# Kernel optimization log

Measured on AMD Instinct MI355X. Metric: run time of the kernel, lower is better.

The kernel has to match this reference:

```python
import jax, jax.numpy as jnp
import numpy as np

N = 100_000
E = 1_600_000
E_OUT = 400_000
IN_DIM = 16
HID = 128
OUT_DIM = 2
L = 6
BN_EPS = 1e-5


def setup_inputs() -> dict:
    key = jax.random.key(0)
    ks = jax.random.split(key, 8)
    x = jax.random.normal(ks[0], (N, IN_DIM), dtype=jnp.float32)
    edge_index = jax.random.randint(ks[1], (2, E), 0, N, dtype=jnp.int32)
    edge_index_out = jax.random.randint(ks[2], (2, E_OUT), 0, N, dtype=jnp.int32)
    embed_W = jax.random.normal(ks[3], (IN_DIM, HID), jnp.float32) / np.sqrt(IN_DIM)
    embed_b = jnp.zeros((HID,), jnp.float32)
    conv_W = jax.random.normal(ks[4], (L, HID, HID), jnp.float32) / np.sqrt(HID)
    conv_b = jnp.zeros((L, HID), jnp.float32)
    bn_gamma = jnp.ones((L, HID), jnp.float32)
    bn_beta = jnp.zeros((L, HID), jnp.float32)
    layer_weights = jnp.ones((L,), jnp.float32)
    fc_W = jax.random.normal(ks[5], (2 * HID, OUT_DIM), jnp.float32) / np.sqrt(2 * HID)
    fc_b = jnp.zeros((OUT_DIM,), jnp.float32)
    return dict(x=x, edge_index=edge_index, edge_index_out=edge_index_out,
                embed_W=embed_W, embed_b=embed_b, conv_W=conv_W, conv_b=conv_b,
                bn_gamma=bn_gamma, bn_beta=bn_beta, layer_weights=layer_weights,
                fc_W=fc_W, fc_b=fc_b)


def reference(x, edge_index, edge_index_out, embed_W, embed_b, conv_W, conv_b,
              bn_gamma, bn_beta, layer_weights, fc_W, fc_b):
    n = x.shape[0]
    # PyG GCNConv default: add self-loops + symmetric normalization
    loops = jnp.arange(n, dtype=edge_index.dtype)
    src = jnp.concatenate([edge_index[0], loops])
    dst = jnp.concatenate([edge_index[1], loops])
    deg = jax.ops.segment_sum(jnp.ones_like(src, jnp.float32), dst, num_segments=n)
    deg_inv_sqrt = jnp.where(deg > 0, jax.lax.rsqrt(jnp.maximum(deg, 1.0)), 0.0)
    norm = (deg_inv_sqrt[src] * deg_inv_sqrt[dst])[:, None]  # [E+N, 1]

    x_embed = x @ embed_W + embed_b  # [N, HID]
    w = jax.nn.softmax(layer_weights)  # softmax=True path

    for i in range(L):
        h = x_embed @ conv_W[i]                                   # linear
        agg = jax.ops.segment_sum(h[src] * norm, dst, num_segments=n) + conv_b[i]
        # BatchNorm1d, training mode (biased variance)
        mean = jnp.mean(agg, axis=0)
        var = jnp.mean(jnp.square(agg - mean), axis=0)
        hbn = (agg - mean) * jax.lax.rsqrt(var + BN_EPS) * bn_gamma[i] + bn_beta[i]
        x_embed = x_embed + w[i] * jax.nn.relu(hbn)               # weighted residual

    edge_repr = jnp.concatenate([x_embed[edge_index_out[0]], x_embed[edge_index_out[1]]], axis=-1)
    return edge_repr @ fc_W + fc_b
```

## Files before the change

### kernel.cpp

```cpp
#include <hip/hip_runtime.h>


#define NW 8192
#define BKT 128
#define CAP 6144
#define CHUNK 512

typedef __attribute__((ext_vector_type(8))) short short8;
typedef __attribute__((ext_vector_type(4))) float f32x4;

static __device__ __forceinline__ unsigned short f2bf(float f) {
  unsigned u = __float_as_uint(f);
  u = u + 0x7fffu + ((u >> 16) & 1u);
  return (unsigned short)(u >> 16);
}
static __device__ __forceinline__ float bf2f_lo(unsigned v) {
  return __uint_as_float(v << 16);
}
static __device__ __forceinline__ float bf2f_hi(unsigned v) {
  return __uint_as_float(v & 0xffff0000u);
}
static __device__ __forceinline__ unsigned pack_bf2(float a, float b) {
  return (unsigned)f2bf(a) | ((unsigned)f2bf(b) << 16);
}
static __device__ __forceinline__ unsigned rfl(unsigned v) {
  return (unsigned)__builtin_amdgcn_readfirstlane((int)v);
}


__global__ __launch_bounds__(256) void hist_bucket_kernel(const int* __restrict__ dst,
                                                          int* __restrict__ bcnt,
                                                          int e, int n, int nbk) {
  __shared__ int h[1024];
  int T = e + n;
  int chunk = (T + gridDim.x - 1) / gridDim.x;
  int j0 = blockIdx.x * chunk;
  int j1 = min(j0 + chunk, T);
  for (int i = threadIdx.x; i < nbk; i += 256) h[i] = 0;
  __syncthreads();
  for (int j = j0 + threadIdx.x; j < j1; j += 256) {
    int d = (j < e) ? dst[j] : (j - e);
    atomicAdd(&h[d >> 7], 1);
  }
  __syncthreads();
  for (int i = threadIdx.x; i < nbk; i += 256)
    if (h[i]) atomicAdd(&bcnt[i], h[i]);
}

__global__ __launch_bounds__(1024) void scan_buckets_kernel(const int* __restrict__ bcnt,
                                                            int* __restrict__ bbase,
                                                            int nbk, int total) {
  __shared__ int lds[1024];
  int t = threadIdx.x;
  int v = (t < nbk) ? bcnt[t] : 0;
  int val = v;
  lds[t] = val; __syncthreads();
  for (int off = 1; off < 1024; off <<= 1) {
    int x = (t >= off) ? lds[t - off] : 0;
    __syncthreads();
    val += x;
    lds[t] = val;
    __syncthreads();
  }
  if (t < nbk) bbase[t] = val - v;
  if (t == 0) bbase[nbk] = total;
}

__global__ __launch_bounds__(256) void scatter_bucket_kernel(const int* __restrict__ src,
                                                             const int* __restrict__ dst,
                                                             int* __restrict__ bfill,
                                                             unsigned* __restrict__ ebuf,
                                                             int e, int n, int nbk) {
  __shared__ int cntL[1024], baseL[1024];
  int T = e + n;
  int chunk = (T + gridDim.x - 1) / gridDim.x;
  int j0 = blockIdx.x * chunk;
  int j1 = min(j0 + chunk, T);
  for (int i = threadIdx.x; i < nbk; i += 256) cntL[i] = 0;
  __syncthreads();
  for (int j = j0 + threadIdx.x; j < j1; j += 256) {
    int d = (j < e) ? dst[j] : (j - e);
    atomicAdd(&cntL[d >> 7], 1);
  }
  __syncthreads();
  for (int i = threadIdx.x; i < nbk; i += 256) {
    int c = cntL[i];
    baseL[i] = c ? atomicAdd(&bfill[i], c) : 0;
    cntL[i] = 0;
  }
  __syncthreads();
  for (int j = j0 + threadIdx.x; j < j1; j += 256) {
    int s, d;
    if (j < e) { s = src[j]; d = dst[j]; } else { s = j - e; d = s; }
    int b = d >> 7;
    int r = atomicAdd(&cntL[b], 1);
    ebuf[baseL[b] + r] = ((unsigned)s << 7) | (unsigned)(d & 127);
  }
}

__global__ __launch_bounds__(256) void sort_bucket_kernel(const int* __restrict__ bbase,
                                                          const unsigned* __restrict__ ebuf,
                                                          int2* __restrict__ ebuf2,
                                                          int* __restrict__ rs,
                                                          float* __restrict__ dis,
                                                          int n, int total) {
  __shared__ unsigned el[CAP];
  __shared__ int hist[BKT], excl[BKT], cur[BKT], scn[BKT];
  int b = blockIdx.x, t = threadIdx.x;
  int e0 = bbase[b], e1 = bbase[b + 1];
  int sz = e1 - e0;
  bool inl = (sz <= CAP);
  if (inl)
    for (int i = t; i < sz; i += 256) el[i] = ebuf[e0 + i];
  if (t < BKT) hist[t] = 0;
  __syncthreads();
  for (int i = t; i < sz; i += 256) {
    unsigned w = inl ? el[i] : ebuf[e0 + i];
    atomicAdd(&hist[w & (BKT - 1)], 1);
  }
  __syncthreads();
  int val = (t < BKT) ? hist[t] : 0;
  if (t < BKT) scn[t] = val;
  __syncthreads();
  for (int off = 1; off < BKT; off <<= 1) {
    int x = (t >= off && t < BKT) ? scn[t - off] : 0;
    __syncthreads();
    if (t < BKT) { val += x; scn[t] = val; }
    __syncthreads();
  }
  if (t < BKT) {
    int ex = val - hist[t];
    excl[t] = ex;
    cur[t] = 0;
    int d = (b << 7) + t;
    if (d < n) {
      rs[d] = e0 + ex;
      dis[d] = rsqrtf((float)hist[t]);
    }
  }
  if (b == 0 && t == 0) rs[n] = total;
  __syncthreads();
  for (int i = t; i < sz; i += 256) {
    unsigned w = inl ? el[i] : ebuf[e0 + i];
    int dl = (int)(w & (BKT - 1));
    int pos = atomicAdd(&cur[dl], 1);
    ebuf2[e0 + excl[dl] + pos] = make_int2((int)(w >> 7), (b << 7) | dl);
  }
}

__global__ void norm_kernel(const int2* __restrict__ ebuf2, const float* __restrict__ dis,
                            int2* __restrict__ esn, int T) {
  int j = blockIdx.x * blockDim.x + threadIdx.x;
  if (j >= T) return;
  int2 p = ebuf2[j];
  float nm = dis[p.x] * dis[p.y];
  unsigned bits = __float_as_uint(nm) & 0xfffffffeu;
  if (j + 1 == T || ebuf2[j + 1].y != p.y) bits |= 1u;
  esn[j] = make_int2(p.x, (int)bits);
}

__global__ void misc_kernel(const int* __restrict__ rs, int* __restrict__ A,
                            int n, int nw, int eb, int wbBlocks,
                            const float* __restrict__ W, unsigned short* __restrict__ Wt,
                            int wtotal, int wtBlocks,
                            const float* __restrict__ lw, float* __restrict__ wsm, int l) {
  int b = blockIdx.x;
  if (b < wbBlocks) {
    int w = b * 256 + threadIdx.x;
    if (w > nw) return;
    int target = w * eb;
    int lo = 0, hi = n;
    while (lo < hi) {
      int mid = (lo + hi) >> 1;
      if (rs[mid] < target) lo = mid + 1; else hi = mid;
    }
    A[w] = lo;
  } else if (b < wbBlocks + wtBlocks) {
    int t = (b - wbBlocks) * 256 + threadIdx.x;
    if (t >= wtotal) return;
    int ll = t >> 14;
    int nc = (t >> 7) & 127;
    int kk = t & 127;
    Wt[t] = f2bf(W[(size_t)ll * 16384 + kk * 128 + nc]);
  } else if (threadIdx.x == 0) {
    float m = lw[0];
    for (int i = 1; i < l; ++i) m = fmaxf(m, lw[i]);
    float s = 0.f;
    for (int i = 0; i < l; ++i) s += expf(lw[i] - m);
    for (int i = 0; i < l; ++i) wsm[i] = expf(lw[i] - m) / s;
  }
}


__global__ __launch_bounds__(256) void embed_kernel(const float* __restrict__ x,
                                                    const float* __restrict__ W,
                                                    const float* __restrict__ b,
                                                    unsigned short* __restrict__ xe16, int n) {
  __shared__ float xs[64][20];
  int tid = threadIdx.x;
  int c = tid & 127, half = tid >> 7;
  float wreg[16];
#pragma unroll
  for (int k = 0; k < 16; ++k) wreg[k] = W[k * 128 + c];
  float bc = b[c];
  int ntile = (n + 63) >> 6;
  for (int t = blockIdx.x; t < ntile; t += gridDim.x) {
    int row0 = t * 64;
    {
      int r = tid >> 2, q = tid & 3;
      int row = row0 + r;
      float4 v = (row < n) ? *(const float4*)(x + (size_t)row * 16 + q * 4)
                           : make_float4(0.f, 0.f, 0.f, 0.f);
      *(float4*)&xs[r][q * 4] = v;
    }
    __syncthreads();
    int rbase = half * 32;
    for (int rr = 0; rr < 32; ++rr) {
      int row = row0 + rbase + rr;
      if (row >= n) break;
      float acc = bc;
#pragma unroll
      for (int k = 0; k < 16; ++k) acc = fmaf(xs[rbase + rr][k], wreg[k], acc);
      xe16[(size_t)row * 128 + c] = f2bf(acc);
    }
    __syncthreads();
  }
}


#define EPS 132

template<bool HASBN>
__global__ __launch_bounds__(256) void gemm_fused_kernel(
    const unsigned* __restrict__ aggbf,
    const float* __restrict__ stats8,
    const float* __restrict__ gamma, const float* __restrict__ beta,
    const float* __restrict__ wsm, int layer,
    unsigned* __restrict__ xe16,
    const unsigned short* __restrict__ Wt,
    unsigned char* __restrict__ Hq,
    float* __restrict__ hscale, int n) {
  __shared__ short8 wlds[2048];
  __shared__ unsigned short ep[64 * EPS];
  __shared__ float sc_s[128], sh_s[128];
  int tid = threadIdx.x;
  const short* WtS = (const short*)Wt;
#pragma unroll
  for (int it = 0; it < 8; ++it) {
    int s = it * 256 + tid;
    int ln = s & 63, g = s >> 6;
    int col = ((g >> 2) << 4) + (ln & 15);
    wlds[s] = *(const short8*)(WtS + (size_t)col * 128 + (g & 3) * 32 + (ln >> 4) * 8);
  }
  if (HASBN && tid < 128) {
    float s = 0.f, q = 0.f;
#pragma unroll
    for (int k = 0; k < 8; ++k) {
      s += stats8[k * 256 + tid];
      q += stats8[k * 256 + 128 + tid];
    }
    float invn = 1.f / (float)n;
    float mean = s * invn;
    float var = q * invn - mean * mean;
    float sc = gamma[tid] * rsqrtf(var + 1e-5f);
    sc_s[tid] = sc;
    sh_s[tid] = beta[tid] - mean * sc;
  }
  __syncthreads();

  int wid = tid >> 6, lane = tid & 63;
  int lrow = lane & 15, lk = lane >> 4;
  float wres = HASBN ? wsm[layer] : 0.f;

  int ntiles = (n + 63) >> 6;
  for (int tile = blockIdx.x; tile < ntiles; tile += gridDim.x) {
    int row = tile * 64 + wid * 16 + lrow;
    short8 afrag[4];
    if (row < n) {
      if (HASBN) {
        const unsigned* arow = aggbf + (size_t)row * 64;
        unsigned* xrow = xe16 + (size_t)row * 64;
#pragma unroll
        for (int ks = 0; ks < 4; ++ks) {
          int c0 = ks * 32 + lk * 8;
          uint4 av = *(const uint4*)(arow + (c0 >> 1));
          uint4 xw = *(const uint4*)(xrow + (c0 >> 1));
          unsigned aw[4] = {av.x, av.y, av.z, av.w};
          unsigned xv[4] = {xw.x, xw.y, xw.z, xw.w};
          unsigned xo[4];
          short8 af;
#pragma unroll
          for (int d = 0; d < 4; ++d) {
            int c = c0 + 2 * d;
            float v0 = fmaxf(fmaf(bf2f_lo(aw[d]), sc_s[c], sh_s[c]), 0.f);
            float v1 = fmaxf(fmaf(bf2f_hi(aw[d]), sc_s[c + 1], sh_s[c + 1]), 0.f);
            float xn0 = fmaf(wres, v0, bf2f_lo(xv[d]));
            float xn1 = fmaf(wres, v1, bf2f_hi(xv[d]));
            unsigned pw = pack_bf2(xn0, xn1);
            xo[d] = pw;
            af[2 * d]     = (short)(pw & 0xffff);
            af[2 * d + 1] = (short)(pw >> 16);
          }
          *(uint4*)(xrow + (c0 >> 1)) = make_uint4(xo[0], xo[1], xo[2], xo[3]);
          afrag[ks] = af;
        }
      } else {
        const short* AS = (const short*)xe16;
#pragma unroll
        for (int ks = 0; ks < 4; ++ks)
          afrag[ks] = *(const short8*)(AS + (size_t)row * 128 + ks * 32 + lk * 8);
      }
    } else {
#pragma unroll
      for (int ks = 0; ks < 4; ++ks) afrag[ks] = (short8)0;
    }
    f32x4 acc[8];
#pragma unroll
    for (int n0 = 0; n0 < 8; ++n0) acc[n0] = (f32x4)0.f;
#pragma unroll
    for (int ks = 0; ks < 4; ++ks)
#pragma unroll
      for (int n0 = 0; n0 < 8; ++n0)
        acc[n0] = __builtin_amdgcn_mfma_f32_16x16x32_bf16(
            afrag[ks], wlds[(n0 * 4 + ks) * 64 + lane], acc[n0], 0, 0, 0);

    int eprow0 = wid * 16 + lk * 4;
#pragma unroll
    for (int n0 = 0; n0 < 8; ++n0) {
      int col = n0 * 16 + lrow;
#pragma unroll
      for (int r = 0; r < 4; ++r)
        ep[(eprow0 + r) * EPS + col] = f2bf(acc[n0][r]);
    }
    __syncthreads();
    int trow = tid >> 2;
    int tchunk = tid & 3;
    int orow = tile * 64 + trow;
    const unsigned short* srcl = ep + trow * EPS + tchunk * 32;
    float vals[32];
    float mx = 0.f;
#pragma unroll
    for (int c = 0; c < 4; ++c) {
      short8 ch = *(const short8*)(srcl + c * 8);
#pragma unroll
      for (int i = 0; i < 8; ++i) {
        float v = __uint_as_float(((unsigned)(unsigned short)ch[i]) << 16);
        vals[c * 8 + i] = v;
        mx = fmaxf(mx, __builtin_fabsf(v));
      }
    }
    mx = fmaxf(mx, __shfl_xor(mx, 1));
    mx = fmaxf(mx, __shfl_xor(mx, 2));
    float inv = (mx > 0.f) ? 127.f / mx : 0.f;
    if (orow < n) {
      if (tchunk == 0) hscale[orow] = mx * (1.f / 127.f);
      unsigned q[8];
#pragma unroll
      for (int d = 0; d < 8; ++d) {
        unsigned b = 0;
#pragma unroll
        for (int j = 0; j < 4; ++j) {
          int qi = (int)rintf(vals[d * 4 + j] * inv);
          b |= ((unsigned)(qi & 0xff)) << (8 * j);
        }
        q[d] = b;
      }
      uint4* dst = (uint4*)(Hq + (size_t)orow * 128 + tchunk * 32);
      dst[0] = make_uint4(q[0], q[1], q[2], q[3]);
      dst[1] = make_uint4(q[4], q[5], q[6], q[7]);
    }
    __syncthreads();
  }
}


#define SPMM_STEP(SW, VI)                                                  \
  {                                                                        \
    float fac = __uint_as_float(((SW) & 0x7ffeu) << 16);                   \
    a0 = fmaf(fac, (float)(signed char)((VI) & 0xff), a0);                 \
    a1 = fmaf(fac, (float)(signed char)((VI) >> 8), a1);                   \
    if ((SW) & 1u) {                                                       \
      aggbf[(size_t)row * 64 + lane] = pack_bf2(a0, a1);                   \
      t0 += a0; t1 += a1;                                                  \
      u0 = fmaf(a0, a0, u0); u1 = fmaf(a1, a1, u1);                        \
      a0 = 0.f; a1 = 0.f;                                                  \
      ++row;                                                               \
    }                                                                      \
  }

#define SPMM_GATHER(SW) (*(const unsigned short*)(hqb + (((SW) >> 8) & ~127u) + lane2))

__global__ __launch_bounds__(256) void spmm_kernel(
    const int* __restrict__ rs, const int* __restrict__ A,
    const int2* __restrict__ esn, const float* __restrict__ hscale,
    const unsigned char* __restrict__ hq,
    unsigned* __restrict__ aggbf, float* __restrict__ stats8, int n) {
  __shared__ unsigned lrec[4][CHUNK];
  int tid = threadIdx.x;
  int wid = tid >> 6, lane = tid & 63;
  int lane2 = lane * 2;
  const char* hqb = (const char*)hq;
  unsigned* lr = lrec[wid];
  int w = blockIdx.x * 4 + wid;
  int row = __builtin_amdgcn_readfirstlane(A[w]);
  int row_end = __builtin_amdgcn_readfirstlane(A[w + 1]);
  float t0 = 0.f, t1 = 0.f, u0 = 0.f, u1 = 0.f;
  if (row < row_end) {
    int e0 = __builtin_amdgcn_readfirstlane(rs[row]);
    int eend = __builtin_amdgcn_readfirstlane(rs[row_end]);
    float a0 = 0.f, a1 = 0.f;
    for (int base = e0; base < eend; base += CHUNK) {
      int cnt = min(CHUNK, eend - base);
      for (int i = lane; i < cnt; i += 64) {
        int2 p = esn[base + i];
        unsigned bits = (unsigned)p.y;
        float f = __uint_as_float(bits & 0xfffffffeu) * hscale[p.x];
        unsigned fb = __float_as_uint(f) + 0x10000u;
        lr[i] = ((unsigned)p.x << 15) | (((fb >> 17) & 0x3fffu) << 1) | (bits & 1u);
      }
      __asm__ volatile("s_waitcnt lgkmcnt(0)" ::: "memory");
      int i = 0;
      for (; i + 8 <= cnt; i += 8) {
        uint4 qa = *(const uint4*)(lr + i);
        uint4 qb = *(const uint4*)(lr + i + 4);
        unsigned w0 = rfl(qa.x), w1 = rfl(qa.y), w2 = rfl(qa.z), w3 = rfl(qa.w);
        unsigned w4 = rfl(qb.x), w5 = rfl(qb.y), w6 = rfl(qb.z), w7 = rfl(qb.w);
        unsigned v0 = SPMM_GATHER(w0);
        unsigned v1 = SPMM_GATHER(w1);
        unsigned v2 = SPMM_GATHER(w2);
        unsigned v3 = SPMM_GATHER(w3);
        unsigned v4 = SPMM_GATHER(w4);
        unsigned v5 = SPMM_GATHER(w5);
        unsigned v6 = SPMM_GATHER(w6);
        unsigned v7 = SPMM_GATHER(w7);
        SPMM_STEP(w0, v0) SPMM_STEP(w1, v1)
        SPMM_STEP(w2, v2) SPMM_STEP(w3, v3)
        SPMM_STEP(w4, v4) SPMM_STEP(w5, v5)
        SPMM_STEP(w6, v6) SPMM_STEP(w7, v7)
      }
      for (; i < cnt; ++i) {
        unsigned sw = rfl(lr[i]);
        unsigned v = SPMM_GATHER(sw);
        SPMM_STEP(sw, v)
      }
      __asm__ volatile("" ::: "memory");
    }
  }
  __shared__ float red[4][256];
  red[0][tid] = t0; red[1][tid] = t1; red[2][tid] = u0; red[3][tid] = u1;
  __syncthreads();
  float v = red[wid][lane] + red[wid][64 + lane] + red[wid][128 + lane] + red[wid][192 + lane];
  int c = (wid == 0) ? (2 * lane) : (wid == 1) ? (2 * lane + 1)
        : (wid == 2) ? (128 + 2 * lane) : (129 + 2 * lane);
  atomicAdd(&stats8[(blockIdx.x & 7) * 256 + c], v);
}


__global__ __launch_bounds__(256) void fc_node_kernel(
    const unsigned* __restrict__ aggbf, const float* __restrict__ stats8,
    const float* __restrict__ gamma, const float* __restrict__ beta,
    const float* __restrict__ wsm, int layer,
    const unsigned* __restrict__ xe16, const float* __restrict__ fcW,
    float* __restrict__ y, int n) {
  __shared__ float sc_s[128], sh_s[128];
  int tid = threadIdx.x;
  if (tid < 128) {
    float s = 0.f, q = 0.f;
#pragma unroll
    for (int k = 0; k < 8; ++k) {
      s += stats8[k * 256 + tid];
      q += stats8[k * 256 + 128 + tid];
    }
    float invn = 1.f / (float)n;
    float mean = s * invn;
    float var = q * invn - mean * mean;
    float sc = gamma[tid] * rsqrtf(var + 1e-5f);
    sc_s[tid] = sc;
    sh_s[tid] = beta[tid] - mean * sc;
  }
  __syncthreads();
  int wid = tid >> 6, lane = tid & 63;
  int r = blockIdx.x * 4 + wid;
  if (r >= n) return;
  float w = wsm[layer];
  unsigned av = aggbf[(size_t)r * 64 + lane];
  unsigned xv = xe16[(size_t)r * 64 + lane];
  int c0 = lane * 2, c1 = c0 + 1;
  float x0 = fmaf(w, fmaxf(fmaf(bf2f_lo(av), sc_s[c0], sh_s[c0]), 0.f), bf2f_lo(xv));
  float x1 = fmaf(w, fmaxf(fmaf(bf2f_hi(av), sc_s[c1], sh_s[c1]), 0.f), bf2f_hi(xv));
  float a00 = x0 * fcW[c0 * 2 + 0] + x1 * fcW[c1 * 2 + 0];
  float a01 = x0 * fcW[c0 * 2 + 1] + x1 * fcW[c1 * 2 + 1];
  float a10 = x0 * fcW[(128 + c0) * 2 + 0] + x1 * fcW[(128 + c1) * 2 + 0];
  float a11 = x0 * fcW[(128 + c0) * 2 + 1] + x1 * fcW[(128 + c1) * 2 + 1];
#pragma unroll
  for (int off = 32; off; off >>= 1) {
    a00 += __shfl_down(a00, off);
    a01 += __shfl_down(a01, off);
    a10 += __shfl_down(a10, off);
    a11 += __shfl_down(a11, off);
  }
  if (lane == 0) *(float4*)(y + (size_t)r * 4) = make_float4(a00, a01, a10, a11);
}

__global__ void edge_out_kernel(const float* __restrict__ y, const int* __restrict__ eo,
                                const float* __restrict__ fcb, float* __restrict__ out, int m) {
  int j = blockIdx.x * blockDim.x + threadIdx.x;
  if (j >= m) return;
  int a = eo[j], b = eo[m + j];
  float4 ya = *(const float4*)(y + (size_t)a * 4);
  float4 yb = *(const float4*)(y + (size_t)b * 4);
  out[(size_t)j * 2 + 0] = ya.x + yb.z + fcb[0];
  out[(size_t)j * 2 + 1] = ya.y + yb.w + fcb[1];
}


extern "C" void kernel_launch(void* const* d_in, const int* in_sizes, int n_in,
                              void* d_out, int out_size, void* d_ws, size_t ws_size,
                              hipStream_t stream) {
  const float* x     = (const float*)d_in[0];
  const int*   ei    = (const int*)d_in[1];
  const int*   eo    = (const int*)d_in[2];
  const float* embW  = (const float*)d_in[3];
  const float* embB  = (const float*)d_in[4];
  const float* convW = (const float*)d_in[5];
  const float* gamma = (const float*)d_in[7];
  const float* beta  = (const float*)d_in[8];
  const float* lw    = (const float*)d_in[9];
  const float* fcW   = (const float*)d_in[10];
  const float* fcb   = (const float*)d_in[11];
  float* out = (float*)d_out;

  const int n = in_sizes[0] / 16;
  const int e = in_sizes[1] / 2;
  const int m = in_sizes[2] / 2;
  const int L = in_sizes[5] / (128 * 128);

  const int T   = e + n;
  const int EB  = (T + NW - 1) / NW;
  const int nbk = (n + BKT - 1) / BKT;

  const int* esrc = ei;
  const int* edst = ei + e;

  char* wsp = (char*)d_ws;
  size_t off = 0;
  auto take = [&](size_t bytes) -> void* {
    void* p = wsp + off;
    off = (off + bytes + 255) & ~(size_t)255;
    return p;
  };
  int*            bcnt     = (int*)take((size_t)(nbk + 1) * 4);
  int*            bbase    = (int*)take((size_t)(nbk + 1) * 4);
  int*            bfill    = (int*)take((size_t)(nbk + 1) * 4);
  int*            rs       = (int*)take((size_t)(n + 1) * 4);
  float*          dis      = (float*)take((size_t)n * 4);
  float*          hscale   = (float*)take((size_t)n * 4);
  float*          wsm      = (float*)take(64 * 4);
  float*          stats    = (float*)take((size_t)L * 8 * 256 * 4);
  int*            A        = (int*)take((size_t)(NW + 1) * 4);
  unsigned*       ebuf     = (unsigned*)take((size_t)T * 4);
  int2*           ebuf2    = (int2*)take((size_t)T * 8);
  int2*           esn      = (int2*)take((size_t)T * 8);
  unsigned short* xe16     = (unsigned short*)take((size_t)n * 128 * 2);
  unsigned char*  hq       = (unsigned char*)take((size_t)n * 128);
  unsigned*       aggbf    = (unsigned*)take((size_t)n * 64 * 4);
  unsigned short* Wt       = (unsigned short*)take((size_t)L * 128 * 128 * 2);
  float*          y        = (float*)take((size_t)n * 4 * 4);
  if (off > ws_size || nbk > 1024) return;

  hipMemsetAsync(bcnt, 0, (size_t)(nbk + 1) * 4, stream);
  hipMemsetAsync(stats, 0, (size_t)L * 8 * 256 * 4, stream);
  hist_bucket_kernel<<<512, 256, 0, stream>>>(edst, bcnt, e, n, nbk);
  scan_buckets_kernel<<<1, 1024, 0, stream>>>(bcnt, bbase, nbk, T);
  hipMemcpyAsync(bfill, bbase, (size_t)nbk * 4, hipMemcpyDeviceToDevice, stream);
  scatter_bucket_kernel<<<512, 256, 0, stream>>>(esrc, edst, bfill, ebuf, e, n, nbk);
  sort_bucket_kernel<<<nbk, 256, 0, stream>>>(bbase, ebuf, ebuf2, rs, dis, n, T);
  norm_kernel<<<(T + 255) / 256, 256, 0, stream>>>(ebuf2, dis, esn, T);
  const int wbBlocks = (NW + 256) / 256;
  const int wtBlocks = (L * 16384 + 255) / 256;
  misc_kernel<<<wbBlocks + wtBlocks + 1, 256, 0, stream>>>(
      rs, A, n, NW, EB, wbBlocks, convW, Wt, L * 16384, wtBlocks, lw, wsm, L);

  embed_kernel<<<1024, 256, 0, stream>>>(x, embW, embB, xe16, n);

  const int ntiles = (n + 63) >> 6;
  const int gemm_grid = (ntiles + 1) / 2;
  for (int i = 0; i < L; ++i) {
    if (i == 0) {
      gemm_fused_kernel<false><<<gemm_grid, 256, 0, stream>>>(
          nullptr, nullptr, nullptr, nullptr, wsm, 0, (unsigned*)xe16,
          Wt, hq, hscale, n);
    } else {
      gemm_fused_kernel<true><<<gemm_grid, 256, 0, stream>>>(
          aggbf, stats + (size_t)(i - 1) * 2048,
          gamma + (size_t)(i - 1) * 128, beta + (size_t)(i - 1) * 128, wsm, i - 1,
          (unsigned*)xe16, Wt + (size_t)i * 16384, hq, hscale, n);
    }
    spmm_kernel<<<NW / 4, 256, 0, stream>>>(rs, A, esn, hscale, hq,
                                            aggbf, stats + (size_t)i * 2048, n);
  }

  fc_node_kernel<<<(n + 3) / 4, 256, 0, stream>>>(
      aggbf, stats + (size_t)(L - 1) * 2048,
      gamma + (size_t)(L - 1) * 128, beta + (size_t)(L - 1) * 128, wsm, L - 1,
      (const unsigned*)xe16, fcW, y, n);
  edge_out_kernel<<<(m + 255) / 256, 256, 0, stream>>>(y, eo, fcb, out, m);
}
```

Baseline: 560.0 us.

## Double-buffer SpMM edge-record staging with register prefetch of next chunks

```diff
diff --git a/kernel.cpp b/kernel.cpp
--- a/kernel.cpp
+++ b/kernel.cpp
@@ -5,6 +5,7 @@
 #define BKT 128
 #define CAP 6144
 #define CHUNK 512
+#define JPW 8
 
 typedef __attribute__((ext_vector_type(8))) short short8;
 typedef __attribute__((ext_vector_type(4))) float f32x4;
@@ -395,12 +396,11 @@
     const int2* __restrict__ esn, const float* __restrict__ hscale,
     const unsigned char* __restrict__ hq,
     unsigned* __restrict__ aggbf, float* __restrict__ stats8, int n) {
-  __shared__ unsigned lrec[4][CHUNK];
+  __shared__ unsigned lrec[4][2][CHUNK];
   int tid = threadIdx.x;
   int wid = tid >> 6, lane = tid & 63;
   int lane2 = lane * 2;
   const char* hqb = (const char*)hq;
-  unsigned* lr = lrec[wid];
   int w = blockIdx.x * 4 + wid;
   int row = __builtin_amdgcn_readfirstlane(A[w]);
   int row_end = __builtin_amdgcn_readfirstlane(A[w + 1]);
@@ -409,20 +409,48 @@
     int e0 = __builtin_amdgcn_readfirstlane(rs[row]);
     int eend = __builtin_amdgcn_readfirstlane(rs[row_end]);
     float a0 = 0.f, a1 = 0.f;
-    for (int base = e0; base < eend; base += CHUNK) {
-      int cnt = min(CHUNK, eend - base);
-      for (int i = lane; i < cnt; i += 64) {
-        int2 p = esn[base + i];
-        unsigned bits = (unsigned)p.y;
-        float f = __uint_as_float(bits & 0xfffffffeu) * hscale[p.x];
-        unsigned fb = __float_as_uint(f) + 0x10000u;
-        lr[i] = ((unsigned)p.x << 15) | (((fb >> 17) & 0x3fffu) << 1) | (bits & 1u);
+
+    int basek = e0;
+    int cntk = min(CHUNK, eend - basek);
+    unsigned* cur = lrec[wid][0];
+    unsigned* nxt = lrec[wid][1];
+    for (int i = lane; i < cntk; i += 64) {
+      int2 p = esn[basek + i];
+      unsigned bits = (unsigned)p.y;
+      float f = __uint_as_float(bits & 0xfffffffeu) * hscale[p.x];
+      unsigned fb = __float_as_uint(f) + 0x10000u;
+      cur[i] = ((unsigned)p.x << 15) | (((fb >> 17) & 0x3fffu) << 1) | (bits & 1u);
+    }
+    int basen = basek + cntk;
+    int cntn = (basen < eend) ? min(CHUNK, eend - basen) : 0;
+    int2 pr[JPW];
+#pragma unroll
+    for (int j = 0; j < JPW; ++j) {
+      int i = lane + j * 64;
+      if (i < cntn) pr[j] = esn[basen + i];
+    }
+
+    while (cntk > 0) {
+      float sr[JPW];
+      int2 pr2[JPW];
+      int basenn = basen + cntn;
+      int cntnn = (cntn > 0 && basenn < eend) ? min(CHUNK, eend - basenn) : 0;
+#pragma unroll
+      for (int j = 0; j < JPW; ++j) {
+        int i = lane + j * 64;
+        if (i < cntn) sr[j] = hscale[pr[j].x];
+      }
+#pragma unroll
+      for (int j = 0; j < JPW; ++j) {
+        int i = lane + j * 64;
+        if (i < cntnn) pr2[j] = esn[basenn + i];
       }
       __asm__ volatile("s_waitcnt lgkmcnt(0)" ::: "memory");
+
       int i = 0;
-      for (; i + 8 <= cnt; i += 8) {
-        uint4 qa = *(const uint4*)(lr + i);
-        uint4 qb = *(const uint4*)(lr + i + 4);
+      for (; i + 8 <= cntk; i += 8) {
+        uint4 qa = *(const uint4*)(cur + i);
+        uint4 qb = *(const uint4*)(cur + i + 4);
         unsigned w0 = rfl(qa.x), w1 = rfl(qa.y), w2 = rfl(qa.z), w3 = rfl(qa.w);
         unsigned w4 = rfl(qb.x), w5 = rfl(qb.y), w6 = rfl(qb.z), w7 = rfl(qb.w);
         unsigned v0 = SPMM_GATHER(w0);
@@ -438,12 +466,29 @@
         SPMM_STEP(w4, v4) SPMM_STEP(w5, v5)
         SPMM_STEP(w6, v6) SPMM_STEP(w7, v7)
       }
-      for (; i < cnt; ++i) {
-        unsigned sw = rfl(lr[i]);
+      for (; i < cntk; ++i) {
+        unsigned sw = rfl(cur[i]);
         unsigned v = SPMM_GATHER(sw);
         SPMM_STEP(sw, v)
       }
-      __asm__ volatile("" ::: "memory");
+
+      if (cntn > 0) {
+#pragma unroll
+        for (int j = 0; j < JPW; ++j) {
+          int i2 = lane + j * 64;
+          if (i2 < cntn) {
+            unsigned bits = (unsigned)pr[j].y;
+            float f = __uint_as_float(bits & 0xfffffffeu) * sr[j];
+            unsigned fb = __float_as_uint(f) + 0x10000u;
+            nxt[i2] = ((unsigned)pr[j].x << 15) | (((fb >> 17) & 0x3fffu) << 1) | (bits & 1u);
+          }
+        }
+      }
+      unsigned* tmp = cur; cur = nxt; nxt = tmp;
+      basek = basen; cntk = cntn;
+      basen = basenn; cntn = cntnn;
+#pragma unroll
+      for (int j = 0; j < JPW; ++j) pr[j] = pr2[j];
     }
   }
   __shared__ float red[4][256];
```

Measured after the change: 636.7 us. 13.7% more time.
